# Optimization experiments

Measured on AMD Instinct MI355X. Metric: run time of the kernel, lower is better.

## Reference

```python
import jax, jax.numpy as jnp
import numpy as np

B, T, F, H = 64, 1024, 512, 512


def setup_inputs() -> dict:
    key = jax.random.key(0)
    k1, k2, k3 = jax.random.split(key, 3)
    scale_x = 1.0 / np.sqrt(F)
    scale_h = 1.0 / np.sqrt(H)
    inputs = jax.random.normal(k1, (B, T, F), dtype=jnp.float32)
    Wx = jax.random.normal(k2, (F, 4 * H), dtype=jnp.float32) * scale_x
    Wh = jax.random.normal(k3, (H, 4 * H), dtype=jnp.float32) * scale_h
    # flax LSTMCell inits forget-gate bias to ones, others zero (gate order i,f,g,o)
    b = jnp.concatenate([jnp.zeros((H,)), jnp.ones((H,)), jnp.zeros((2 * H,))]).astype(jnp.float32)
    return {"inputs": inputs, "Wx": Wx, "Wh": Wh, "b": b}


def reference(inputs, Wx, Wh, b):
    """LSTM encoder: scan LSTMCell over time, return final carry (c, h).

    inputs: [B, T, F]; Wx: [F, 4H]; Wh: [H, 4H]; b: [4H].
    Gate order i, f, g, o (matches flax.nn.LSTMCell).
    """
    Bx = inputs.shape[0]
    Hh = Wh.shape[0]
    # Precompute input projections for all timesteps in one big GEMM: [T, B, 4H]
    x_proj = jnp.einsum('btf,fg->tbg', inputs, Wx) + b

    def step(carry, xp_t):
        c, h = carry
        gates = xp_t + h @ Wh  # [B, 4H]
        i, f, g, o = jnp.split(gates, 4, axis=-1)
        i = jax.nn.sigmoid(i)
        f = jax.nn.sigmoid(f)
        g = jnp.tanh(g)
        o = jax.nn.sigmoid(o)
        c_new = f * c + i * g
        h_new = o * jnp.tanh(c_new)
        return (c_new, h_new), None

    c0 = jnp.zeros((Bx, Hh), dtype=inputs.dtype)
    h0 = jnp.zeros((Bx, Hh), dtype=inputs.dtype)
    (c_fin, h_fin), _ = jax.lax.scan(step, (c0, h0), x_proj)
    return c_fin, h_fin
```

## Files before the change

kernel.cpp:

```cpp
#include <hip/hip_runtime.h>
#include <hip/hip_fp16.h>

#define T_DIM 1024
#define B_DIM 64
#define F_DIM 512
#define H_DIM 512
#define G4    2048
#define HSZ   (B_DIM*H_DIM)

typedef _Float16 h16;
typedef unsigned long long u64;
typedef _Float16 v8h __attribute__((ext_vector_type(8)));
typedef _Float16 v4h __attribute__((ext_vector_type(4)));
typedef _Float16 v2h __attribute__((ext_vector_type(2)));
typedef float    v4f __attribute__((ext_vector_type(4)));
typedef unsigned v4u __attribute__((ext_vector_type(4)));
typedef unsigned v2u __attribute__((ext_vector_type(2)));

#define NGRP   8
#define GROWS  8
#define GWORDS 2048
#define NWG    128
#define WSTEPS 16
#define DESC_OFF  ((size_t)2*NGRP*GWORDS)
#define TRIAL_OFF (DESC_OFF + NWG)
#define VOTE_OFF  (TRIAL_OFF + NWG)
#define ABORT_OFF (VOTE_OFF + NWG)

#define XP_HALVES ((size_t)T_DIM * 256 * 2 * 64 * 4)
#define XP_BYTES  (XP_HALVES * 2)
#define HB_WORDS  (ABORT_OFF + NGRP)
#define HB_BYTES  (HB_WORDS * 8)
#define X16_BYTES ((size_t)B_DIM * T_DIM * F_DIM * 2)
#define WXP_BYTES ((size_t)G4 * F_DIM * 2)

__global__ __launch_bounds__(256) void conv_x_kernel(
    const float* __restrict__ X, h16* __restrict__ X16)
{
  const size_t total4 = (size_t)B_DIM * T_DIM * F_DIM / 4;
  for (size_t i = blockIdx.x * 256 + threadIdx.x; i < total4;
       i += (size_t)gridDim.x * 256) {
    float4 v = ((const float4*)X)[i];
    v4h w = { (h16)v.x, (h16)v.y, (h16)v.z, (h16)v.w };
    ((v4h*)X16)[i] = w;
  }
}

__global__ __launch_bounds__(256) void conv_w_kernel(
    const float* __restrict__ Wx, h16* __restrict__ Wxp)
{
  const int gid = blockIdx.x * 256 + threadIdx.x;
  const int pcg = gid >> 6;
  const int k8  = gid & 63;
  const int ub  = pcg >> 5, Tt = (pcg >> 4) & 1, nn = pcg & 15;
  const int gcol = (Tt*2 + (nn >> 3))*512 + ub*8 + (nn & 7);
  v8h w;
  #pragma unroll
  for (int j = 0; j < 8; ++j)
    w[j] = (h16)Wx[(size_t)(k8*8 + j)*G4 + gcol];
  *(v8h*)(Wxp + (size_t)pcg*512 + k8*8) = w;
}

__global__ __launch_bounds__(256) void xproj_kernel(
    const h16* __restrict__ X16, const h16* __restrict__ Wxp,
    const float* __restrict__ bias, h16* __restrict__ xp)
{
  __shared__ __align__(16) h16 As[128*72];
  __shared__ __align__(16) h16 Bs[128*72];
  const int wgid = blockIdx.x;
  const int wgn  = wgid & 15;
  const int bg   = (wgid >> 4) & 3;
  const int t0   = (wgid >> 6) * 8;
  const int tid  = threadIdx.x;
  const int lane = tid & 63;
  const int wv   = tid >> 6;
  const int mh   = wv & 1, nh = wv >> 1;
  const int n    = lane & 15, quad = lane >> 4;

  v4f acc[4][4];
  #pragma unroll
  for (int mi = 0; mi < 4; ++mi)
    #pragma unroll
    for (int ni = 0; ni < 4; ++ni) acc[mi][ni] = {0.f, 0.f, 0.f, 0.f};

  const int m  = tid >> 1;
  const int kh = tid & 1;
  const int abl = m & 15, atl = m >> 4;
  const h16* asrc0 = X16 + ((size_t)(bg*16 + abl)*T_DIM + (t0 + atl))*F_DIM
                         + kh*32;
  const h16* bsrc0 = Wxp + (size_t)(wgn*128 + m)*512 + kh*32;
  h16* adst = As + m*72 + kh*32;
  h16* bdst = Bs + m*72 + kh*32;

  for (int kc = 0; kc < 8; ++kc) {
    __syncthreads();
    {
      const h16* asrc = asrc0 + kc*64;
      const h16* bsrc = bsrc0 + kc*64;
      #pragma unroll
      for (int j = 0; j < 32; j += 8) {
        *(v8h*)(adst + j) = *(const v8h*)(asrc + j);
        *(v8h*)(bdst + j) = *(const v8h*)(bsrc + j);
      }
    }
    __syncthreads();
    #pragma unroll
    for (int kk = 0; kk < 2; ++kk) {
      v8h aF[4], bF[4];
      #pragma unroll
      for (int mi = 0; mi < 4; ++mi)
        aF[mi] = *(const v8h*)(As + ((mh*4 + mi)*16 + n)*72 + kk*32 + quad*8);
      #pragma unroll
      for (int ni = 0; ni < 4; ++ni)
        bF[ni] = *(const v8h*)(Bs + ((nh*4 + ni)*16 + n)*72 + kk*32 + quad*8);
      #pragma unroll
      for (int mi = 0; mi < 4; ++mi)
        #pragma unroll
        for (int ni = 0; ni < 4; ++ni)
          acc[mi][ni] = __builtin_amdgcn_mfma_f32_16x16x32_f16(
              aF[mi], bF[ni], acc[mi][ni], 0, 0, 0);
    }
  }
  #pragma unroll
  for (int ni = 0; ni < 4; ++ni) {
    int pc0  = wgn*128 + (nh*4 + ni)*16;
    int ub   = pc0 >> 5, Tt = (pc0 >> 4) & 1;
    int gcol = (Tt*2 + (n >> 3))*512 + ub*8 + (n & 7);
    float bv = bias[gcol];
    int wg2  = bg*64 + ub;
    #pragma unroll
    for (int mi = 0; mi < 4; ++mi) {
      int t = t0 + mh*4 + mi;
      size_t off = ((((size_t)t*256 + wg2)*2 + Tt)*256) + lane*4;
      v4h o = { (h16)(acc[mi][ni][0] + bv), (h16)(acc[mi][ni][1] + bv),
                (h16)(acc[mi][ni][2] + bv), (h16)(acc[mi][ni][3] + bv) };
      *(v4h*)(xp + off) = o;
    }
  }
}

__device__ __forceinline__ float fsig(float x) {
  return __builtin_amdgcn_rcpf(1.f + __expf(-x));
}
__device__ __forceinline__ float ftanh(float x) {
  return 1.f - 2.f * __builtin_amdgcn_rcpf(__expf(2.f*x) + 1.f);
}

__device__ __forceinline__ u64 load_nt_u64(const u64* p) {
  v2u r;
  asm volatile("global_load_dwordx2 %0, %1, off nt\n\ts_waitcnt vmcnt(0)"
               : "=v"(r) : "v"(p) : "memory");
  return ((u64)r.y << 32) | (u64)r.x;
}

__global__ __launch_bounds__(256, 1) void scan_kernel(
    const float* __restrict__ Wh, const h16* __restrict__ xp,
    u64* __restrict__ hbuf, float* __restrict__ out)
{
  const int bx   = blockIdx.x;
  const int tid  = threadIdx.x;
  const int wv   = tid >> 6;
  const int lane = tid & 63;
  const int n    = lane & 15, quad = lane >> 4;

  __shared__ __align__(16) unsigned hlds[2][2052];
  __shared__ __align__(16) unsigned char xs[4*8192];
  __shared__ float gbuf[4][16*33];
  __shared__ unsigned char xcds[NWG];
  __shared__ unsigned char pos2bx[NWG];
  __shared__ int sflag[2];

  unsigned xcd;
  asm volatile("s_getreg_b32 %0, hwreg(20, 0, 32)" : "=s"(xcd));
  xcd &= 7u;
  u64* const desc = hbuf + DESC_OFF;
  if (tid == 0)
    __hip_atomic_store(desc + bx, ((u64)0xABu << 56) | (u64)xcd,
                       __ATOMIC_RELAXED, __HIP_MEMORY_SCOPE_AGENT);
  if (tid < NWG) {
    u64 d = __hip_atomic_load(desc + tid, __ATOMIC_RELAXED,
                              __HIP_MEMORY_SCOPE_AGENT);
    while ((unsigned)(d >> 56) != 0xABu) {
      __builtin_amdgcn_s_sleep(1);
      d = __hip_atomic_load(desc + tid, __ATOMIC_RELAXED,
                            __HIP_MEMORY_SCOPE_AGENT);
    }
    xcds[tid] = (unsigned char)(d & 7u);
  }
  if (tid < 4) { hlds[0][2048 + tid] = 0; hlds[1][2048 + tid] = 0; }
  __syncthreads();

  int start = 0, cnt = 0, rank = 0;
  for (int i = 0; i < NWG; ++i) {
    const int x = xcds[i];
    start += (x < (int)xcd) ? 1 : 0;
    cnt   += (x == (int)xcd) ? 1 : 0;
    rank  += (x == (int)xcd && i < bx) ? 1 : 0;
  }
  const int pos = start + rank;
  const int g = pos >> 4, w = pos & 15;
  bool fast = (g*16 >= start) && (g*16 + 16 <= start + cnt);

  if (fast) {
    if (tid < NWG) {
      const int xi = xcds[tid];
      int st = 0, rk = 0;
      for (int i = 0; i < NWG; ++i) {
        const int x = xcds[i];
        st += (x < xi) ? 1 : 0;
        rk += (x == xi && i < tid) ? 1 : 0;
      }
      pos2bx[st + rk] = (unsigned char)tid;
    }
    __syncthreads();
    u64* const trial = hbuf + TRIAL_OFF;
    u64* const vote  = hbuf + VOTE_OFF;
    if (tid == 0)
      __hip_atomic_store(trial + bx, ((u64)0xCDu << 56) | (u64)bx,
                         __ATOMIC_RELAXED, __HIP_MEMORY_SCOPE_WORKGROUP);
    int seen = 1;
    if (tid < 16) {
      const int tb = pos2bx[g*16 + tid];
      const u64 want = ((u64)0xCDu << 56) | (u64)tb;
      seen = 0;
      for (int it = 0; it < 1024; ++it) {
        if (load_nt_u64(trial + tb) == want) { seen = 1; break; }
        __builtin_amdgcn_s_sleep(1);
      }
    }
    if (tid < 64) {
      const int okw = __all(seen);
      if (tid == 0) sflag[0] = okw;
    }
    __syncthreads();
    if (tid == 0)
      __hip_atomic_store(vote + bx, ((u64)0xEFu << 56) | (u64)(sflag[0] & 1),
                         __ATOMIC_RELAXED, __HIP_MEMORY_SCOPE_AGENT);
    int vok = 1;
    if (tid < 16) {
      const int tb = pos2bx[g*16 + tid];
      u64 d = __hip_atomic_load(vote + tb, __ATOMIC_RELAXED,
                                __HIP_MEMORY_SCOPE_AGENT);
      while ((unsigned)(d >> 56) != 0xEFu) {
        __builtin_amdgcn_s_sleep(1);
        d = __hip_atomic_load(vote + tb, __ATOMIC_RELAXED,
                              __HIP_MEMORY_SCOPE_AGENT);
      }
      vok = (int)(d & 1);
    }
    if (tid < 64) {
      const int allv = __all(vok);
      if (tid == 0) sflag[1] = allv;
    }
    __syncthreads();
    fast = (sflag[1] != 0);
  }

  const int ub  = w*4 + wv;
  const int u0  = ub*8;
  const int g01 = n >> 3;
  const int uc  = u0 + (n & 7);

  v8h bF0[16], bF1[16];
  #pragma unroll
  for (int kk = 0; kk < 16; ++kk) {
    const int kb = kk*32 + quad*8;
    v8h f0, f1;
    #pragma unroll
    for (int j = 0; j < 8; ++j) {
      f0[j] = (h16)Wh[(size_t)(kb + j)*G4 + (g01*512 + uc)];
      f1[j] = (h16)Wh[(size_t)(kb + j)*G4 + ((2 + g01)*512 + uc)];
    }
    bF0[kk] = f0; bF1[kk] = f1;
  }

  float c0 = 0.f, c1 = 0.f, hf0 = 0.f, hf1 = 0.f;

  const bool act = (n < GROWS);
  const int  pW  = ub*32 + n*4 + quad;
  u64* const gbase0 = hbuf + (size_t)g * GWORDS;
  u64* const gbase1 = hbuf + (size_t)(NGRP + g) * GWORDS;
  u64* const abw    = hbuf + ABORT_OFF + g;
  u64* const gb0p   = gbase0 + pW;
  u64* const gb1p   = gbase1 + pW;
  u64 lw0 = 0, lw1 = 0;

  const int bgrp = g >> 1;
  const int gp   = g & 1;
  unsigned char* const xsw = xs + wv*8192;

  int pslot[8], pchunk[8], pk[8];
  #pragma unroll
  for (int j = 0; j < 8; ++j) {
    const int p2 = j*64 + lane;
    pslot[j]  = p2 >> 5;
    pchunk[j] = (p2 >> 4) & 1;
    pk[j]     = p2 & 15;
  }
  v4u rg[8];
  #pragma unroll
  for (int j = 0; j < 8; ++j) {
    const size_t ubase = ((size_t)pslot[j]*256 + bgrp*64 + ub)*512;
    rg[j] = *(const v4u*)(xp + ubase + gp*128 + pchunk[j]*256 + pk[j]*8);
  }

  const int hbase = act ? (quad*32 + n*4) : 2048;
  const int hoff  = act ? 128 : 0;

  for (int t = 0; t < T_DIM; ++t) {
    const int p = t & 1;
    const int s = t & 15;

    u64* const hb = (p ? gbase1 : gbase0) + tid*2;
    const unsigned target = (unsigned)t;
    unsigned pay0, pay1, pay2, pay3, pay4, pay5, pay6, pay7;
    bool got = false;

    if (fast) {
      const u64* a0 = hb;
      const u64* a1 = hb + 512;
      const u64* a2 = hb + 1024;
      const u64* a3 = hb + 1536;
      int rounds = 0;
      for (;;) {
        v4u q0, q1, q2, q3;
        asm volatile("global_load_dwordx4 %0, %1, off nt"
                     : "=v"(q0) : "v"(a0) : "memory");
        asm volatile("global_load_dwordx4 %0, %1, off nt"
                     : "=v"(q1) : "v"(a1) : "memory");
        asm volatile("global_load_dwordx4 %0, %1, off nt"
                     : "=v"(q2) : "v"(a2) : "memory");
        asm volatile("global_load_dwordx4 %0, %1, off nt"
                     : "=v"(q3) : "v"(a3) : "memory");
        asm volatile("s_waitcnt vmcnt(0)"
                     : "+v"(q0), "+v"(q1), "+v"(q2), "+v"(q3) :: "memory");
        __builtin_amdgcn_sched_barrier(0);
        const unsigned bad = (q0.y ^ target) | (q0.w ^ target)
                           | (q1.y ^ target) | (q1.w ^ target)
                           | (q2.y ^ target) | (q2.w ^ target)
                           | (q3.y ^ target) | (q3.w ^ target);
        if (__all((int)(bad == 0))) {
          pay0 = q0.x; pay1 = q0.z; pay2 = q1.x; pay3 = q1.z;
          pay4 = q2.x; pay5 = q2.z; pay6 = q3.x; pay7 = q3.z;
          got = true;
          break;
        }
        ++rounds;
        if ((rounds & 31) == 16) {
          u64 ab = __hip_atomic_load(abw, __ATOMIC_RELAXED,
                                     __HIP_MEMORY_SCOPE_AGENT);
          if (__any((int)(ab != 0)) || rounds > 512) {
            __hip_atomic_store(abw, (u64)1, __ATOMIC_RELAXED,
                               __HIP_MEMORY_SCOPE_AGENT);
            if (lw0) __hip_atomic_store(gb0p, lw0, __ATOMIC_RELAXED,
                                        __HIP_MEMORY_SCOPE_AGENT);
            if (lw1) __hip_atomic_store(gb1p, lw1, __ATOMIC_RELAXED,
                                        __HIP_MEMORY_SCOPE_AGENT);
            fast = false;
            break;
          }
        }
        if (rounds > 4) __builtin_amdgcn_s_sleep(1);
      }
    }
    if (!got) {
      for (;;) {
        u64 wq[8];
        #pragma unroll
        for (int j = 0; j < 4; ++j) {
          wq[j*2]   = __hip_atomic_load(hb + j*512,     __ATOMIC_RELAXED,
                                        __HIP_MEMORY_SCOPE_AGENT);
          wq[j*2+1] = __hip_atomic_load(hb + j*512 + 1, __ATOMIC_RELAXED,
                                        __HIP_MEMORY_SCOPE_AGENT);
        }
        unsigned bad = 0;
        #pragma unroll
        for (int j = 0; j < 8; ++j)
          bad |= ((unsigned)(wq[j] >> 32)) ^ target;
        if (__all((int)(bad == 0))) {
          pay0 = (unsigned)wq[0]; pay1 = (unsigned)wq[1];
          pay2 = (unsigned)wq[2]; pay3 = (unsigned)wq[3];
          pay4 = (unsigned)wq[4]; pay5 = (unsigned)wq[5];
          pay6 = (unsigned)wq[6]; pay7 = (unsigned)wq[7];
          break;
        }
        __builtin_amdgcn_s_sleep(1);
      }
    }

    if (s == 0) {
      #pragma unroll
      for (int j = 0; j < 8; ++j)
        *(v4u*)(xsw + pslot[j]*512 + pchunk[j]*256 + pk[j]*16) = rg[j];
    }

    {
      v2u* hl = (v2u*)hlds[p];
      hl[tid]       = (v2u){pay0, pay1};
      hl[tid + 256] = (v2u){pay2, pay3};
      hl[tid + 512] = (v2u){pay4, pay5};
      hl[tid + 768] = (v2u){pay6, pay7};
    }
    __syncthreads();

    const unsigned char* xb = xsw + s*512 + (quad & 1)*128 + n*8;
    v4h x0 = *(const v4h*)xb;
    v4h x1 = *(const v4h*)(xb + 256);

    v4f acc0 = { (float)x0[0], (float)x0[1], (float)x0[2], (float)x0[3] };
    v4f acc1 = { (float)x1[0], (float)x1[1], (float)x1[2], (float)x1[3] };
    v4f acc2 = { 0.f, 0.f, 0.f, 0.f };
    v4f acc3 = { 0.f, 0.f, 0.f, 0.f };
    const unsigned* hfr = &hlds[p][hbase];
    #pragma unroll
    for (int kk = 0; kk < 8; ++kk) {
      v8h a0 = *(const v8h*)(hfr + kk*hoff);
      v8h a1 = *(const v8h*)(hfr + (kk+8)*hoff);
      acc0 = __builtin_amdgcn_mfma_f32_16x16x32_f16(a0, bF0[kk],   acc0, 0,0,0);
      acc1 = __builtin_amdgcn_mfma_f32_16x16x32_f16(a0, bF1[kk],   acc1, 0,0,0);
      acc2 = __builtin_amdgcn_mfma_f32_16x16x32_f16(a1, bF0[kk+8], acc2, 0,0,0);
      acc3 = __builtin_amdgcn_mfma_f32_16x16x32_f16(a1, bF1[kk+8], acc3, 0,0,0);
    }
    acc0 += acc2; acc1 += acc3;

    float* gb = gbuf[wv];
    #pragma unroll
    for (int r = 0; r < 4; ++r) {
      const int row = quad*4 + r;
      gb[row*33 + n]      = acc0[r];
      gb[row*33 + 16 + n] = acc1[r];
    }
    __builtin_amdgcn_wave_barrier();
    const float* gr = gb + n*33;
    const int ua2 = quad*2;
    float gi0 = gr[ua2],   gf0 = gr[8+ua2], gg0 = gr[16+ua2], go0 = gr[24+ua2];
    float gi1 = gr[ua2+1], gf1 = gr[9+ua2], gg1 = gr[17+ua2], go1 = gr[25+ua2];
    __builtin_amdgcn_wave_barrier();

    gi0 = fsig(gi0); gf0 = fsig(gf0); gg0 = ftanh(gg0); go0 = fsig(go0);
    gi1 = fsig(gi1); gf1 = fsig(gf1); gg1 = ftanh(gg1); go1 = fsig(go1);
    c0 = gf0*c0 + gi0*gg0;  hf0 = go0*ftanh(c0);
    c1 = gf1*c1 + gi1*gg1;  hf1 = go1*ftanh(c1);

    if (t < T_DIM - 1 && act) {
      union { v2h v; unsigned u; } pw;
      pw.v = (v2h){ (h16)hf0, (h16)hf1 };
      const u64 word = ((u64)(unsigned)(t + 1) << 32) | (u64)pw.u;
      u64* const hwp = (p ? gbase0 : gbase1) + pW;
      if (fast) {
        __hip_atomic_store(hwp, word, __ATOMIC_RELAXED,
                           __HIP_MEMORY_SCOPE_WORKGROUP);
        if (p) lw0 = word; else lw1 = word;
      } else {
        __hip_atomic_store(hwp, word, __ATOMIC_RELAXED,
                           __HIP_MEMORY_SCOPE_AGENT);
      }
    }

    if (s == WSTEPS - 1 && t + 1 < T_DIM) {
      const int tw = t + 1;
      #pragma unroll
      for (int j = 0; j < 8; ++j) {
        const size_t ubase = ((size_t)(tw + pslot[j])*256 + bgrp*64 + ub)*512;
        rg[j] = *(const v4u*)(xp + ubase + gp*128 + pchunk[j]*256 + pk[j]*8);
      }
    }
  }

  if (act) {
    float* oc = out + (size_t)(g*GROWS + n)*H_DIM + u0 + quad*2;
    oc[0] = c0; oc[1] = c1;
    oc[HSZ + 0] = hf0; oc[HSZ + 1] = hf1;
  }
}

extern "C" void kernel_launch(void* const* d_in, const int* in_sizes, int n_in,
                              void* d_out, int out_size, void* d_ws, size_t ws_size,
                              hipStream_t stream) {
  const float* X    = (const float*)d_in[0];
  const float* Wx   = (const float*)d_in[1];
  const float* Wh   = (const float*)d_in[2];
  const float* bias = (const float*)d_in[3];
  float* out = (float*)d_out;

  char* ws = (char*)d_ws;
  h16* xp   = (h16*)ws;
  u64* hbuf = (u64*)(ws + XP_BYTES);
  h16* X16  = (h16*)(ws + XP_BYTES + HB_BYTES);
  h16* Wxp  = (h16*)(ws + XP_BYTES + HB_BYTES + X16_BYTES);

  hipMemsetAsync(ws + XP_BYTES, 0, HB_BYTES, stream);

  conv_x_kernel<<<4096, 256, 0, stream>>>(X, X16);
  conv_w_kernel<<<512, 256, 0, stream>>>(Wx, Wxp);
  xproj_kernel<<<8192, 256, 0, stream>>>(X16, Wxp, bias, xp);
  scan_kernel<<<NWG, 256, 0, stream>>>(Wh, xp, hbuf, out);
}
```

Measured before the change: 1.998 ms.

## Replace per-word step tags with per-wave flag counters for hidden-state exchange

Hidden-state exchange between workgroups changes from 64-bit words carrying a step tag, which every consumer polled, to 32-bit payload words plus one monotonic flag per producing wave. Consumers now spin on a single flag dword per lane, then issue one round of payload loads. This halves payload traffic and makes polling cheaper. The cost is an extra serialized round trip (flag, then data) and a vmcnt wait before each flag store, and correctness depends on store ordering across workgroups sharing an L2 scope.

Result: slower. 2.415 ms (+20.9%).

```diff
diff --git a/kernel.cpp b/kernel.cpp
--- a/kernel.cpp
+++ b/kernel.cpp
@@ -19,10 +19,10 @@
 
 #define NGRP   8
 #define GROWS  8
-#define GWORDS 2048
 #define NWG    128
 #define WSTEPS 16
-#define DESC_OFF  ((size_t)2*NGRP*GWORDS)
+#define FLAG32_OFF 32768
+#define DESC_OFF  ((size_t)16640)
 #define TRIAL_OFF (DESC_OFF + NWG)
 #define VOTE_OFF  (TRIAL_OFF + NWG)
 #define ABORT_OFF (VOTE_OFF + NWG)
@@ -170,6 +170,9 @@
   __shared__ unsigned char pos2bx[NWG];
   __shared__ int sflag[2];
 
+  unsigned* const pay = (unsigned*)hbuf;
+  unsigned* const flg = pay + FLAG32_OFF;
+
   unsigned xcd;
   asm volatile("s_getreg_b32 %0, hwreg(20, 0, 32)" : "=s"(xcd));
   xcd &= 7u;
@@ -255,6 +258,7 @@
     __syncthreads();
     fast = (sflag[1] != 0);
   }
+  const bool everfast = fast;
 
   const int ub  = w*4 + wv;
   const int u0  = ub*8;
@@ -278,12 +282,12 @@
 
   const bool act = (n < GROWS);
   const int  pW  = ub*32 + n*4 + quad;
-  u64* const gbase0 = hbuf + (size_t)g * GWORDS;
-  u64* const gbase1 = hbuf + (size_t)(NGRP + g) * GWORDS;
-  u64* const abw    = hbuf + ABORT_OFF + g;
-  u64* const gb0p   = gbase0 + pW;
-  u64* const gb1p   = gbase1 + pW;
-  u64 lw0 = 0, lw1 = 0;
+  unsigned* const pay0b = pay + (size_t)g*2048;
+  unsigned* const pay1b = pay + (size_t)(NGRP + g)*2048;
+  u64* const abw  = hbuf + ABORT_OFF + g;
+  const unsigned* const flagp = flg + g*64 + lane;
+  unsigned* const flagw = flg + g*64 + ub;
+  unsigned lw0 = 0, lw1 = 0, lfv = 0;
 
   const int bgrp = g >> 1;
   const int gp   = g & 1;
@@ -310,80 +314,49 @@
   for (int t = 0; t < T_DIM; ++t) {
     const int p = t & 1;
     const int s = t & 15;
-
-    u64* const hb = (p ? gbase1 : gbase0) + tid*2;
     const unsigned target = (unsigned)t;
-    unsigned pay0, pay1, pay2, pay3, pay4, pay5, pay6, pay7;
-    bool got = false;
 
     if (fast) {
-      const u64* a0 = hb;
-      const u64* a1 = hb + 512;
-      const u64* a2 = hb + 1024;
-      const u64* a3 = hb + 1536;
       int rounds = 0;
       for (;;) {
-        v4u q0, q1, q2, q3;
-        asm volatile("global_load_dwordx4 %0, %1, off nt"
-                     : "=v"(q0) : "v"(a0) : "memory");
-        asm volatile("global_load_dwordx4 %0, %1, off nt"
-                     : "=v"(q1) : "v"(a1) : "memory");
-        asm volatile("global_load_dwordx4 %0, %1, off nt"
-                     : "=v"(q2) : "v"(a2) : "memory");
-        asm volatile("global_load_dwordx4 %0, %1, off nt"
-                     : "=v"(q3) : "v"(a3) : "memory");
-        asm volatile("s_waitcnt vmcnt(0)"
-                     : "+v"(q0), "+v"(q1), "+v"(q2), "+v"(q3) :: "memory");
-        __builtin_amdgcn_sched_barrier(0);
-        const unsigned bad = (q0.y ^ target) | (q0.w ^ target)
-                           | (q1.y ^ target) | (q1.w ^ target)
-                           | (q2.y ^ target) | (q2.w ^ target)
-                           | (q3.y ^ target) | (q3.w ^ target);
-        if (__all((int)(bad == 0))) {
-          pay0 = q0.x; pay1 = q0.z; pay2 = q1.x; pay3 = q1.z;
-          pay4 = q2.x; pay5 = q2.z; pay6 = q3.x; pay7 = q3.z;
-          got = true;
-          break;
-        }
+        unsigned fv;
+        asm volatile("global_load_dword %0, %1, off nt\n\ts_waitcnt vmcnt(0)"
+                     : "=v"(fv) : "v"(flagp) : "memory");
+        if (__all((int)(fv >= target))) break;
         ++rounds;
-        if ((rounds & 31) == 16) {
+        if ((rounds & 31) == 0) {
           u64 ab = __hip_atomic_load(abw, __ATOMIC_RELAXED,
                                      __HIP_MEMORY_SCOPE_AGENT);
-          if (__any((int)(ab != 0)) || rounds > 512) {
+          if (__any((int)(ab != 0)) || rounds > 1024) {
             __hip_atomic_store(abw, (u64)1, __ATOMIC_RELAXED,
                                __HIP_MEMORY_SCOPE_AGENT);
-            if (lw0) __hip_atomic_store(gb0p, lw0, __ATOMIC_RELAXED,
-                                        __HIP_MEMORY_SCOPE_AGENT);
-            if (lw1) __hip_atomic_store(gb1p, lw1, __ATOMIC_RELAXED,
-                                        __HIP_MEMORY_SCOPE_AGENT);
+            if (act) {
+              __hip_atomic_store(pay0b + pW, lw0, __ATOMIC_RELAXED,
+                                 __HIP_MEMORY_SCOPE_AGENT);
+              __hip_atomic_store(pay1b + pW, lw1, __ATOMIC_RELAXED,
+                                 __HIP_MEMORY_SCOPE_AGENT);
+            }
+            asm volatile("s_waitcnt vmcnt(0)" ::: "memory");
+            if (lane == 0)
+              __hip_atomic_store(flagw, lfv, __ATOMIC_RELAXED,
+                                 __HIP_MEMORY_SCOPE_AGENT);
             fast = false;
             break;
           }
         }
-        if (rounds > 4) __builtin_amdgcn_s_sleep(1);
-      }
-    }
-    if (!got) {
+        if (rounds > 8) __builtin_amdgcn_s_sleep(1);
+      }
+    }
+    if (!fast) {
+      int rounds = 0;
       for (;;) {
-        u64 wq[8];
-        #pragma unroll
-        for (int j = 0; j < 4; ++j) {
-          wq[j*2]   = __hip_atomic_load(hb + j*512,     __ATOMIC_RELAXED,
+        unsigned fv = __hip_atomic_load(flagp, __ATOMIC_RELAXED,
                                         __HIP_MEMORY_SCOPE_AGENT);
-          wq[j*2+1] = __hip_atomic_load(hb + j*512 + 1, __ATOMIC_RELAXED,
-                                        __HIP_MEMORY_SCOPE_AGENT);
-        }
-        unsigned bad = 0;
-        #pragma unroll
-        for (int j = 0; j < 8; ++j)
-          bad |= ((unsigned)(wq[j] >> 32)) ^ target;
-        if (__all((int)(bad == 0))) {
-          pay0 = (unsigned)wq[0]; pay1 = (unsigned)wq[1];
-          pay2 = (unsigned)wq[2]; pay3 = (unsigned)wq[3];
-          pay4 = (unsigned)wq[4]; pay5 = (unsigned)wq[5];
-          pay6 = (unsigned)wq[6]; pay7 = (unsigned)wq[7];
-          break;
-        }
+        if (__all((int)(fv >= target))) break;
+        ++rounds;
+        if ((rounds & 63) == 0 && lane == 0)
+          __hip_atomic_store(abw, (u64)1, __ATOMIC_RELAXED,
+                             __HIP_MEMORY_SCOPE_AGENT);
         __builtin_amdgcn_s_sleep(1);
       }
     }
@@ -394,12 +367,43 @@
         *(v4u*)(xsw + pslot[j]*512 + pchunk[j]*256 + pk[j]*16) = rg[j];
     }
 
+    v2u r0, r1, r2, r3;
+    {
+      const unsigned* pb = (p ? pay1b : pay0b) + tid*2;
+      if (fast) {
+        asm volatile("global_load_dwordx2 %0, %1, off nt"
+                     : "=v"(r0) : "v"(pb) : "memory");
+        asm volatile("global_load_dwordx2 %0, %1, off nt"
+                     : "=v"(r1) : "v"(pb + 512) : "memory");
+        asm volatile("global_load_dwordx2 %0, %1, off nt"
+                     : "=v"(r2) : "v"(pb + 1024) : "memory");
+        asm volatile("global_load_dwordx2 %0, %1, off nt"
+                     : "=v"(r3) : "v"(pb + 1536) : "memory");
+        asm volatile("s_waitcnt vmcnt(0)"
+                     : "+v"(r0), "+v"(r1), "+v"(r2), "+v"(r3) :: "memory");
+        __builtin_amdgcn_sched_barrier(0);
+      } else {
+        u64 w0 = __hip_atomic_load((const u64*)(pb),        __ATOMIC_RELAXED,
+                                   __HIP_MEMORY_SCOPE_AGENT);
+        u64 w1 = __hip_atomic_load((const u64*)(pb + 512),  __ATOMIC_RELAXED,
+                                   __HIP_MEMORY_SCOPE_AGENT);
+        u64 w2 = __hip_atomic_load((const u64*)(pb + 1024), __ATOMIC_RELAXED,
+                                   __HIP_MEMORY_SCOPE_AGENT);
+        u64 w3 = __hip_atomic_load((const u64*)(pb + 1536), __ATOMIC_RELAXED,
+                                   __HIP_MEMORY_SCOPE_AGENT);
+        r0 = (v2u){(unsigned)w0, (unsigned)(w0 >> 32)};
+        r1 = (v2u){(unsigned)w1, (unsigned)(w1 >> 32)};
+        r2 = (v2u){(unsigned)w2, (unsigned)(w2 >> 32)};
+        r3 = (v2u){(unsigned)w3, (unsigned)(w3 >> 32)};
+      }
+    }
+
     {
       v2u* hl = (v2u*)hlds[p];
-      hl[tid]       = (v2u){pay0, pay1};
-      hl[tid + 256] = (v2u){pay2, pay3};
-      hl[tid + 512] = (v2u){pay4, pay5};
-      hl[tid + 768] = (v2u){pay6, pay7};
+      hl[tid]       = r0;
+      hl[tid + 256] = r1;
+      hl[tid + 512] = r2;
+      hl[tid + 768] = r3;
     }
     __syncthreads();
 
@@ -442,18 +446,28 @@
     c0 = gf0*c0 + gi0*gg0;  hf0 = go0*ftanh(c0);
     c1 = gf1*c1 + gi1*gg1;  hf1 = go1*ftanh(c1);
 
-    if (t < T_DIM - 1 && act) {
-      union { v2h v; unsigned u; } pw;
-      pw.v = (v2h){ (h16)hf0, (h16)hf1 };
-      const u64 word = ((u64)(unsigned)(t + 1) << 32) | (u64)pw.u;
-      u64* const hwp = (p ? gbase0 : gbase1) + pW;
-      if (fast) {
-        __hip_atomic_store(hwp, word, __ATOMIC_RELAXED,
-                           __HIP_MEMORY_SCOPE_WORKGROUP);
-        if (p) lw0 = word; else lw1 = word;
-      } else {
-        __hip_atomic_store(hwp, word, __ATOMIC_RELAXED,
-                           __HIP_MEMORY_SCOPE_AGENT);
+    if (t < T_DIM - 1) {
+      if (act) {
+        union { v2h v; unsigned u; } pw_;
+        pw_.v = (v2h){ (h16)hf0, (h16)hf1 };
+        unsigned* pp = (p ? pay0b : pay1b) + pW;
+        if (fast)
+          __hip_atomic_store(pp, pw_.u, __ATOMIC_RELAXED,
+                             __HIP_MEMORY_SCOPE_WORKGROUP);
+        else
+          __hip_atomic_store(pp, pw_.u, __ATOMIC_RELAXED,
+                             __HIP_MEMORY_SCOPE_AGENT);
+        if (p) lw0 = pw_.u; else lw1 = pw_.u;
+      }
+      asm volatile("s_waitcnt vmcnt(0)" ::: "memory");
+      lfv = (unsigned)(t + 1);
+      if (lane == 0) {
+        if (fast)
+          __hip_atomic_store(flagw, lfv, __ATOMIC_RELAXED,
+                             __HIP_MEMORY_SCOPE_WORKGROUP);
+        else
+          __hip_atomic_store(flagw, lfv, __ATOMIC_RELAXED,
+                             __HIP_MEMORY_SCOPE_AGENT);
       }
     }
 
@@ -465,6 +479,19 @@
         rg[j] = *(const v4u*)(xp + ubase + gp*128 + pchunk[j]*256 + pk[j]*8);
       }
     }
+  }
+
+  if (everfast) {
+    if (act) {
+      __hip_atomic_store(pay0b + pW, lw0, __ATOMIC_RELAXED,
+                         __HIP_MEMORY_SCOPE_AGENT);
+      __hip_atomic_store(pay1b + pW, lw1, __ATOMIC_RELAXED,
+                         __HIP_MEMORY_SCOPE_AGENT);
+    }
+    asm volatile("s_waitcnt vmcnt(0)" ::: "memory");
+    if (lane == 0)
+      __hip_atomic_store(flagw, lfv, __ATOMIC_RELAXED,
+                         __HIP_MEMORY_SCOPE_AGENT);
   }
 
   if (act) {
```
